# Optimization experiments

Hardware: AMD Instinct MI355X
Metric: run time of the kernel (lower is better)

Reference implementation:

```python
import jax, jax.numpy as jnp
import numpy as np

B, T, C, H = 8, 2048, 1024, 64  # batch, seq (block_size), n_embd, head_size


def setup_inputs() -> dict:
    key = jax.random.key(0)
    kx, kq, kk, kv = jax.random.split(key, 4)
    s = 1.0 / np.sqrt(C)
    return {
        "x": jax.random.normal(kx, (B, T, C), dtype=jnp.float32),
        "Wq": jax.random.normal(kq, (C, H), dtype=jnp.float32) * s,
        "Wk": jax.random.normal(kk, (C, H), dtype=jnp.float32) * s,
        "Wv": jax.random.normal(kv, (C, H), dtype=jnp.float32) * s,
    }


def reference(x, Wq, Wk, Wv):
    t = x.shape[1]
    q = jnp.einsum("btc,ch->bth", x, Wq)
    k = jnp.einsum("btc,ch->bth", x, Wk)
    v = jnp.einsum("btc,ch->bth", x, Wv)
    scores = jnp.einsum("bqh,bkh->bqk", q, k) / jnp.sqrt(jnp.float32(H))
    causal = jnp.tril(jnp.ones((t, t), dtype=bool))  # tril mask
    scores = jnp.where(causal, scores, -jnp.inf)
    attn = jax.nn.softmax(scores, axis=-1)
    return jnp.einsum("bqk,bkh->bqh", attn, v)
```

## Files before the change

### kernel.cpp

```cpp
#include <hip/hip_runtime.h>
#include <hip/hip_bf16.h>

#define BB 8
#define TT 2048
#define CC 1024
#define HH 64
#define NSPLIT 8

typedef __attribute__((ext_vector_type(8)))  short bf16x8;
typedef __attribute__((ext_vector_type(4)))  float f32x4;
typedef __attribute__((ext_vector_type(16))) float f32x16;
typedef __attribute__((ext_vector_type(8)))  unsigned short us8;
typedef unsigned int u32;

static __device__ __forceinline__ unsigned short f2bf(float f) {
    union { float f; unsigned int u; } v; v.f = f;
    unsigned int u = v.u;
    return (unsigned short)((u + 0x7FFFu + ((u >> 16) & 1u)) >> 16);
}
static __device__ __forceinline__ float bf2f(unsigned short s) {
    union { u32 u; float f; } v; v.u = ((u32)s) << 16; return v.f;
}

__global__ __launch_bounds__(256) void prep_weights(
        const float* __restrict__ Wq, const float* __restrict__ Wk,
        const float* __restrict__ Wv, unsigned short* __restrict__ Wt) {
    __shared__ float tile[64][65];
    int w  = blockIdx.x >> 4;
    int c0 = (blockIdx.x & 15) * 64;
    const float* W = (w == 0) ? Wq : (w == 1) ? Wk : Wv;
    int li = threadIdx.x;
    {
        int c = li >> 2, h4 = (li & 3) * 16;
        const float* src = W + (size_t)(c0 + c) * HH + h4;
        #pragma unroll
        for (int i = 0; i < 4; ++i) {
            float4 v4 = *(const float4*)(src + i * 4);
            tile[c][h4 + i*4 + 0] = v4.x; tile[c][h4 + i*4 + 1] = v4.y;
            tile[c][h4 + i*4 + 2] = v4.z; tile[c][h4 + i*4 + 3] = v4.w;
        }
    }
    __syncthreads();
    float scale = (w == 0) ? 0.1803368802f : 1.0f;
    int h = li >> 2, cg = (li & 3) * 16;
    unsigned short* dst = Wt + (size_t)w * HH * CC + (size_t)h * CC + c0 + cg;
    #pragma unroll
    for (int i = 0; i < 16; ++i) dst[i] = f2bf(tile[cg + i][h] * scale);
}

__global__ __launch_bounds__(512, 4) void proj_qkv(
        const float* __restrict__ x, const unsigned short* __restrict__ Wt,
        unsigned short* __restrict__ Pp) {
    __shared__ unsigned short Xs[2][64 * 64];
    __shared__ unsigned short Ws[2][192 * 64];
    int tid = threadIdx.x;
    int wv = tid >> 6, lane = tid & 63;
    int quad = (lane >> 4) & 3, lq = lane & 15;
    int mg = wv >> 2, ng = wv & 3;
    int r0 = blockIdx.x * 64;
    int k0 = blockIdx.y * 512;

    int xr = tid >> 3, xg = tid & 7;
    const float* xsrc = x + (size_t)(r0 + xr) * CC + k0 + xg * 8;
    int xdst = xr * 64 + ((xg ^ (xr & 7)) * 8);
    float4 xa[2], xb[2];

    f32x4 acc[2][3];
    #pragma unroll
    for (int mt = 0; mt < 2; ++mt)
        #pragma unroll
        for (int nt = 0; nt < 3; ++nt)
            #pragma unroll
            for (int i = 0; i < 4; ++i) acc[mt][nt][i] = 0.0f;

    auto stageW = [&](int buf, int kc) {
        #pragma unroll
        for (int i = 0; i < 3; ++i) {
            int fp = tid + i * 512;
            int r = fp >> 3, pb = fp & 7, g = pb ^ (r & 7);
            const u32 __attribute__((address_space(1)))* gsrc =
                (const u32 __attribute__((address_space(1)))*)
                    (Wt + (size_t)r * CC + k0 + kc * 64 + g * 8);
            u32 __attribute__((address_space(3)))* ldst =
                (u32 __attribute__((address_space(3)))*)(&Ws[buf][fp * 8]);
            __builtin_amdgcn_global_load_lds(gsrc, ldst, 16, 0, 0);
        }
    };
    auto loadX = [&](int set, int kc) {
        xa[set] = *(const float4*)(xsrc + kc * 64);
        xb[set] = *(const float4*)(xsrc + kc * 64 + 4);
    };
    auto writeX = [&](int set, int buf) {
        unsigned short h[8];
        h[0]=f2bf(xa[set].x); h[1]=f2bf(xa[set].y);
        h[2]=f2bf(xa[set].z); h[3]=f2bf(xa[set].w);
        h[4]=f2bf(xb[set].x); h[5]=f2bf(xb[set].y);
        h[6]=f2bf(xb[set].z); h[7]=f2bf(xb[set].w);
        *(us8*)&Xs[buf][xdst] = *(const us8*)h;
    };

    loadX(0, 0); loadX(1, 1);
    stageW(0, 0);
    writeX(0, 0);

    for (int kc = 0; kc < 8; ++kc) {
        int cur = kc & 1;
        __syncthreads();
        if (kc < 7) stageW(1 - cur, kc + 1);
        if (kc < 6) loadX(kc & 1, kc + 2);
        #pragma unroll
        for (int ks = 0; ks < 2; ++ks) {
            int g = ks * 4 + quad;
            bf16x8 a[2], b[3];
            #pragma unroll
            for (int mt = 0; mt < 2; ++mt) {
                int arow = mg * 32 + mt * 16 + lq;
                a[mt] = *(const bf16x8*)&Xs[cur][arow * 64 + (g ^ (lq & 7)) * 8];
            }
            #pragma unroll
            for (int nt = 0; nt < 3; ++nt) {
                int brow = ng * 48 + nt * 16 + lq;
                b[nt] = *(const bf16x8*)&Ws[cur][brow * 64 + (g ^ (lq & 7)) * 8];
            }
            #pragma unroll
            for (int mt = 0; mt < 2; ++mt)
                #pragma unroll
                for (int nt = 0; nt < 3; ++nt)
                    acc[mt][nt] = __builtin_amdgcn_mfma_f32_16x16x32_bf16(
                        a[mt], b[nt], acc[mt][nt], 0, 0, 0);
        }
        if (kc < 7) writeX((kc + 1) & 1, 1 - cur);
    }

    unsigned short* Pb =
        Pp + ((size_t)blockIdx.y * (BB * TT) + r0) * 192;
    #pragma unroll
    for (int mt = 0; mt < 2; ++mt) {
        #pragma unroll
        for (int nt = 0; nt < 3; ++nt) {
            int g = ng * 48 + nt * 16 + lq;
            #pragma unroll
            for (int i = 0; i < 4; ++i) {
                int row = mg * 32 + mt * 16 + quad * 4 + i;
                Pb[(size_t)row * 192 + g] = f2bf(acc[mt][nt][i]);
            }
        }
    }
}

__global__ __launch_bounds__(256) void qkv_reduce(
        const unsigned short* __restrict__ Pp,
        unsigned short* __restrict__ qws, unsigned short* __restrict__ kws,
        unsigned short* __restrict__ vws) {
    __shared__ unsigned short Vt[64][72];
    int t = threadIdx.x;
    int br0 = blockIdx.x * 64;
    const size_t H2 = (size_t)BB * TT * 192;
    {
        int r = br0 + (t >> 2), cg = (t & 3) * 32;
        const unsigned short* p0 = Pp + (size_t)r * 192 + cg;
        const unsigned short* p1 = p0 + H2;
        unsigned short* dst = (cg < 64) ? (qws + (size_t)r * HH + cg)
                                        : (kws + (size_t)r * HH + (cg - 64));
        #pragma unroll
        for (int u = 0; u < 4; ++u) {
            us8 a = *(const us8*)(p0 + u * 8);
            us8 b = *(const us8*)(p1 + u * 8);
            unsigned short o[8];
            #pragma unroll
            for (int j = 0; j < 8; ++j) o[j] = f2bf(bf2f(a[j]) + bf2f(b[j]));
            *(us8*)(dst + u * 8) = *(const us8*)o;
        }
    }
    {
        int r = br0 + (t >> 2), ch = (t & 3) * 16;
        const unsigned short* p0 = Pp + (size_t)r * 192 + 128 + ch;
        const unsigned short* p1 = p0 + H2;
        #pragma unroll
        for (int u = 0; u < 2; ++u) {
            us8 a = *(const us8*)(p0 + u * 8);
            us8 b = *(const us8*)(p1 + u * 8);
            #pragma unroll
            for (int j = 0; j < 8; ++j)
                Vt[ch + u * 8 + j][r & 63] = f2bf(bf2f(a[j]) + bf2f(b[j]));
        }
    }
    __syncthreads();
    {
        int h = t >> 2, tb = (t & 3) * 16;
        int b = br0 >> 11, rr = br0 & (TT - 1);
        #pragma unroll
        for (int u = 0; u < 2; ++u)
            *(us8*)(vws + ((size_t)b * HH + h) * TT + rr + tb + u * 8) =
                *(const us8*)&Vt[h][tb + u * 8];
    }
}

__global__ __launch_bounds__(128, 3) void attn(
        const unsigned short* __restrict__ qws,
        const unsigned short* __restrict__ kws,
        const unsigned short* __restrict__ vws,
        unsigned short* __restrict__ Op, float* __restrict__ Lp) {
    __shared__ unsigned short Kt[32][72];
    __shared__ unsigned short Vt[64][40];
    __shared__ unsigned short Ps[64][40];
    int ti = blockIdx.x;
    int s  = blockIdx.y;
    int b  = blockIdx.z;
    int last = 2 * ti + 1;
    if (s > last) return;
    int tid = threadIdx.x, wv = tid >> 6, lane = tid & 63;
    int half = lane >> 5, l31 = lane & 31;

    bf16x8 qf[4];
    {
        const unsigned short* qp =
            qws + ((size_t)b * TT + ti * 64 + wv * 32 + l31) * HH + half * 8;
        #pragma unroll
        for (int ks = 0; ks < 4; ++ks) qf[ks] = *(const bf16x8*)(qp + ks * 16);
    }
    f32x16 O0, O1, Lc;
    #pragma unroll
    for (int i = 0; i < 16; ++i) { O0[i] = 0.f; O1[i] = 0.f; Lc[i] = 0.f; }
    bf16x8 ones;
    #pragma unroll
    for (int i = 0; i < 8; ++i) ones[i] = (short)0x3F80;

    for (int jc = s; jc <= last; jc += NSPLIT) {
        __syncthreads();
        #pragma unroll
        for (int i = 0; i < 2; ++i) {
            int slot = tid + i * 128;
            int r = slot >> 3, g = slot & 7;
            *(us8*)&Kt[r][g * 8] =
                *(const us8*)(kws + ((size_t)b * TT + jc * 32 + r) * HH + g * 8);
        }
        #pragma unroll
        for (int i = 0; i < 2; ++i) {
            int slot = tid + i * 128;
            int h = slot >> 2, kb = slot & 3;
            *(us8*)&Vt[h][kb * 8] =
                *(const us8*)(vws + ((size_t)b * HH + h) * TT + jc * 32 + kb * 8);
        }
        __syncthreads();
        f32x16 S;
        #pragma unroll
        for (int i = 0; i < 16; ++i) S[i] = 0.f;
        #pragma unroll
        for (int ks = 0; ks < 4; ++ks) {
            bf16x8 kf = *(const bf16x8*)&Kt[l31][ks * 16 + half * 8];
            S = __builtin_amdgcn_mfma_f32_32x32x16_bf16(qf[ks], kf, S, 0, 0, 0);
        }
        bool diag = (jc >= 2 * ti + wv);
        #pragma unroll
        for (int r = 0; r < 16; ++r) {
            int pat = (r & 3) + 8 * (r >> 2) + 4 * half;
            float p = __builtin_amdgcn_exp2f(S[r]);
            if (diag && jc * 32 + l31 > ti * 64 + wv * 32 + pat) p = 0.0f;
            Ps[wv * 32 + pat][l31] = f2bf(p);
        }
        #pragma unroll
        for (int ks = 0; ks < 2; ++ks) {
            bf16x8 pa  = *(const bf16x8*)&Ps[wv * 32 + l31][ks * 16 + half * 8];
            bf16x8 vf0 = *(const bf16x8*)&Vt[l31][ks * 16 + half * 8];
            bf16x8 vf1 = *(const bf16x8*)&Vt[32 + l31][ks * 16 + half * 8];
            O0 = __builtin_amdgcn_mfma_f32_32x32x16_bf16(pa, vf0, O0, 0, 0, 0);
            O1 = __builtin_amdgcn_mfma_f32_32x32x16_bf16(pa, vf1, O1, 0, 0, 0);
            Lc = __builtin_amdgcn_mfma_f32_32x32x16_bf16(pa, ones, Lc, 0, 0, 0);
        }
    }
    unsigned short* Ob =
        Op + (((size_t)s * BB + b) * TT + ti * 64 + wv * 32) * HH;
    #pragma unroll
    for (int r = 0; r < 16; ++r) {
        int pat = (r & 3) + 8 * (r >> 2) + 4 * half;
        Ob[(size_t)pat * HH + l31]      = f2bf(O0[r]);
        Ob[(size_t)pat * HH + 32 + l31] = f2bf(O1[r]);
    }
    if (l31 == 0) {
        #pragma unroll
        for (int r = 0; r < 16; ++r) {
            int pat = (r & 3) + 8 * (r >> 2) + 4 * half;
            Lp[((size_t)s * BB + b) * TT + ti * 64 + wv * 32 + pat] = Lc[r];
        }
    }
}

__global__ __launch_bounds__(256) void norm_out(
        const unsigned short* __restrict__ Op, const float* __restrict__ Lp,
        float* __restrict__ out) {
    int idx = blockIdx.x * 256 + threadIdx.x;
    int g = idx >> 2;
    int hseg = (idx & 3) * 16;
    int ti = (g & (TT - 1)) >> 6;
    int ns = min(2 * ti + 2, NSPLIT);
    float a[16];
    #pragma unroll
    for (int j = 0; j < 16; ++j) a[j] = 0.f;
    float Ls = 0.f;
    for (int s = 0; s < ns; ++s) {
        const unsigned short* base =
            Op + ((size_t)s * BB * TT + g) * HH + hseg;
        us8 u0 = *(const us8*)base;
        us8 u1 = *(const us8*)(base + 8);
        #pragma unroll
        for (int j = 0; j < 8; ++j) { a[j] += bf2f(u0[j]); a[8 + j] += bf2f(u1[j]); }
        Ls += Lp[(size_t)s * BB * TT + g];
    }
    float inv = 1.0f / Ls;
    float* ob = out + (size_t)g * HH + hseg;
    #pragma unroll
    for (int q = 0; q < 4; ++q) {
        float4 v = make_float4(a[q*4] * inv, a[q*4+1] * inv,
                               a[q*4+2] * inv, a[q*4+3] * inv);
        ((float4*)ob)[q] = v;
    }
}

extern "C" void kernel_launch(void* const* d_in, const int* in_sizes, int n_in,
                              void* d_out, int out_size, void* d_ws, size_t ws_size,
                              hipStream_t stream) {
    (void)in_sizes; (void)n_in; (void)out_size; (void)ws_size;
    const float* x  = (const float*)d_in[0];
    const float* Wq = (const float*)d_in[1];
    const float* Wk = (const float*)d_in[2];
    const float* Wv = (const float*)d_in[3];
    float* out = (float*)d_out;

    char* ws = (char*)d_ws;
    unsigned short* Wt  = (unsigned short*)ws;
    unsigned short* qws = (unsigned short*)(ws + (1u << 19));
    unsigned short* kws = (unsigned short*)(ws + (1u << 19) + (1u << 21));
    unsigned short* vws = (unsigned short*)(ws + (1u << 19) + (2u << 21));
    unsigned short* Op  = (unsigned short*)(ws + (1u << 19) + (3u << 21));
    float*          Lp  = (float*)(ws + (1u << 19) + (3u << 21) + (1u << 24));
    unsigned short* Pp  = (unsigned short*)(ws + (1u << 19) + (3u << 21)
                                            + (1u << 24) + (1u << 19));

    prep_weights<<<48, 256, 0, stream>>>(Wq, Wk, Wv, Wt);
    proj_qkv<<<dim3(256, 2), 512, 0, stream>>>(x, Wt, Pp);
    qkv_reduce<<<256, 256, 0, stream>>>(Pp, qws, kws, vws);
    attn<<<dim3(32, NSPLIT, 8), 128, 0, stream>>>(qws, kws, vws, Op, Lp);
    norm_out<<<256, 256, 0, stream>>>(Op, Lp, out);
}
```

Measured before the change: 136.9 us.

## Double-buffer 64-key K/V tiles via async global-to-LDS loads with swizzled layout

The attention kernel now processes 64-key tiles instead of 32, and halves the split count. K and V are prefetched into double-buffered shared memory with global_load_lds, so copies overlap with MFMA work. qkv_reduce writes K and V in an XOR-swizzled, tile-blocked layout so the shared-memory fragment reads avoid bank conflicts. Occupancy drops to two blocks per SM to fit the larger shared buffers. There is a risk: the async LDS loads may not be fully waited on before the barrier.

```diff
diff --git a/kernel.cpp b/kernel.cpp
--- a/kernel.cpp
+++ b/kernel.cpp
@@ -5,7 +5,7 @@
 #define TT 2048
 #define CC 1024
 #define HH 64
-#define NSPLIT 8
+#define NSPLIT 4
 
 typedef __attribute__((ext_vector_type(8)))  short bf16x8;
 typedef __attribute__((ext_vector_type(4)))  float f32x4;
@@ -160,8 +160,6 @@
         int r = br0 + (t >> 2), cg = (t & 3) * 32;
         const unsigned short* p0 = Pp + (size_t)r * 192 + cg;
         const unsigned short* p1 = p0 + H2;
-        unsigned short* dst = (cg < 64) ? (qws + (size_t)r * HH + cg)
-                                        : (kws + (size_t)r * HH + (cg - 64));
         #pragma unroll
         for (int u = 0; u < 4; ++u) {
             us8 a = *(const us8*)(p0 + u * 8);
@@ -169,7 +167,13 @@
             unsigned short o[8];
             #pragma unroll
             for (int j = 0; j < 8; ++j) o[j] = f2bf(bf2f(a[j]) + bf2f(b[j]));
-            *(us8*)(dst + u * 8) = *(const us8*)o;
+            if (cg < 64) {
+                *(us8*)(qws + (size_t)r * HH + cg + u * 8) = *(const us8*)o;
+            } else {
+                int gb = ((cg - 64) >> 3) + u;
+                int pb = gb ^ (r & 7);
+                *(us8*)(kws + (size_t)r * HH + pb * 8) = *(const us8*)o;
+            }
         }
     }
     {
@@ -188,27 +192,28 @@
     __syncthreads();
     {
         int h = t >> 2, tb = (t & 3) * 16;
-        int b = br0 >> 11, rr = br0 & (TT - 1);
-        #pragma unroll
-        for (int u = 0; u < 2; ++u)
-            *(us8*)(vws + ((size_t)b * HH + h) * TT + rr + tb + u * 8) =
-                *(const us8*)&Vt[h][tb + u * 8];
-    }
-}
-
-__global__ __launch_bounds__(128, 3) void attn(
+        int b = br0 >> 11, jc = (br0 & (TT - 1)) >> 6;
+        unsigned short* base = vws + (((size_t)b * 32 + jc) * 64 + h) * 64;
+        #pragma unroll
+        for (int u = 0; u < 2; ++u) {
+            int gb = (t & 3) * 2 + u;
+            int pb = gb ^ (h & 7);
+            *(us8*)(base + pb * 8) = *(const us8*)&Vt[h][tb + u * 8];
+        }
+    }
+}
+
+__global__ __launch_bounds__(128, 2) void attn(
         const unsigned short* __restrict__ qws,
         const unsigned short* __restrict__ kws,
         const unsigned short* __restrict__ vws,
         unsigned short* __restrict__ Op, float* __restrict__ Lp) {
-    __shared__ unsigned short Kt[32][72];
-    __shared__ unsigned short Vt[64][40];
-    __shared__ unsigned short Ps[64][40];
+    __shared__ unsigned short KV[16384 + 64 * 66];
+    unsigned short* Ps = &KV[16384];
     int ti = blockIdx.x;
     int s  = blockIdx.y;
     int b  = blockIdx.z;
-    int last = 2 * ti + 1;
-    if (s > last) return;
+    if (s > ti) return;
     int tid = threadIdx.x, wv = tid >> 6, lane = tid & 63;
     int half = lane >> 5, l31 = lane & 31;
 
@@ -226,48 +231,65 @@
     #pragma unroll
     for (int i = 0; i < 8; ++i) ones[i] = (short)0x3F80;
 
-    for (int jc = s; jc <= last; jc += NSPLIT) {
+    auto stageKV = [&](int buf, int jc) {
+        const unsigned short* kbase = kws + ((size_t)b * TT + jc * 64) * HH;
+        const unsigned short* vbase = vws + (((size_t)b * 32 + jc) * 64) * 64;
+        #pragma unroll
+        for (int u = 0; u < 4; ++u) {
+            int f = u * 128 + tid;
+            const u32 __attribute__((address_space(1)))* gk =
+                (const u32 __attribute__((address_space(1)))*)(kbase + f * 8);
+            u32 __attribute__((address_space(3)))* lk =
+                (u32 __attribute__((address_space(3)))*)(&KV[buf * 4096 + f * 8]);
+            __builtin_amdgcn_global_load_lds(gk, lk, 16, 0, 0);
+            const u32 __attribute__((address_space(1)))* gv =
+                (const u32 __attribute__((address_space(1)))*)(vbase + f * 8);
+            u32 __attribute__((address_space(3)))* lv =
+                (u32 __attribute__((address_space(3)))*)(&KV[8192 + buf * 4096 + f * 8]);
+            __builtin_amdgcn_global_load_lds(gv, lv, 16, 0, 0);
+        }
+    };
+
+    stageKV(0, s);
+    int buf = 0;
+    for (int jc = s; jc <= ti; jc += NSPLIT) {
         __syncthreads();
-        #pragma unroll
-        for (int i = 0; i < 2; ++i) {
-            int slot = tid + i * 128;
-            int r = slot >> 3, g = slot & 7;
-            *(us8*)&Kt[r][g * 8] =
-                *(const us8*)(kws + ((size_t)b * TT + jc * 32 + r) * HH + g * 8);
-        }
-        #pragma unroll
-        for (int i = 0; i < 2; ++i) {
-            int slot = tid + i * 128;
-            int h = slot >> 2, kb = slot & 3;
-            *(us8*)&Vt[h][kb * 8] =
-                *(const us8*)(vws + ((size_t)b * HH + h) * TT + jc * 32 + kb * 8);
-        }
-        __syncthreads();
-        f32x16 S;
-        #pragma unroll
-        for (int i = 0; i < 16; ++i) S[i] = 0.f;
+        if (jc + NSPLIT <= ti) stageKV(1 - buf, jc + NSPLIT);
+        const unsigned short* Kc = &KV[buf * 4096];
+        const unsigned short* Vc = &KV[8192 + buf * 4096];
+        f32x16 S[2];
+        #pragma unroll
+        for (int i = 0; i < 16; ++i) { S[0][i] = 0.f; S[1][i] = 0.f; }
+        #pragma unroll
+        for (int nt = 0; nt < 2; ++nt)
+            #pragma unroll
+            for (int ks = 0; ks < 4; ++ks) {
+                int row = nt * 32 + l31, gb = ks * 2 + half;
+                bf16x8 kf = *(const bf16x8*)&Kc[row * 64 + (gb ^ (row & 7)) * 8];
+                S[nt] = __builtin_amdgcn_mfma_f32_32x32x16_bf16(
+                    qf[ks], kf, S[nt], 0, 0, 0);
+            }
+        bool diag = (jc == ti);
+        #pragma unroll
+        for (int nt = 0; nt < 2; ++nt)
+            #pragma unroll
+            for (int r = 0; r < 16; ++r) {
+                int pat = (r & 3) + 8 * (r >> 2) + 4 * half;
+                float p = __builtin_amdgcn_exp2f(S[nt][r]);
+                if (diag && nt * 32 + l31 > wv * 32 + pat) p = 0.0f;
+                Ps[(wv * 32 + pat) * 66 + nt * 32 + l31] = f2bf(p);
+            }
         #pragma unroll
         for (int ks = 0; ks < 4; ++ks) {
-            bf16x8 kf = *(const bf16x8*)&Kt[l31][ks * 16 + half * 8];
-            S = __builtin_amdgcn_mfma_f32_32x32x16_bf16(qf[ks], kf, S, 0, 0, 0);
-        }
-        bool diag = (jc >= 2 * ti + wv);
-        #pragma unroll
-        for (int r = 0; r < 16; ++r) {
-            int pat = (r & 3) + 8 * (r >> 2) + 4 * half;
-            float p = __builtin_amdgcn_exp2f(S[r]);
-            if (diag && jc * 32 + l31 > ti * 64 + wv * 32 + pat) p = 0.0f;
-            Ps[wv * 32 + pat][l31] = f2bf(p);
-        }
-        #pragma unroll
-        for (int ks = 0; ks < 2; ++ks) {
-            bf16x8 pa  = *(const bf16x8*)&Ps[wv * 32 + l31][ks * 16 + half * 8];
-            bf16x8 vf0 = *(const bf16x8*)&Vt[l31][ks * 16 + half * 8];
-            bf16x8 vf1 = *(const bf16x8*)&Vt[32 + l31][ks * 16 + half * 8];
+            int gb = ks * 2 + half;
+            bf16x8 pa = *(const bf16x8*)&Ps[(wv * 32 + l31) * 66 + ks * 16 + half * 8];
+            bf16x8 vf0 = *(const bf16x8*)&Vc[l31 * 64 + (gb ^ (l31 & 7)) * 8];
+            bf16x8 vf1 = *(const bf16x8*)&Vc[(32 + l31) * 64 + (gb ^ (l31 & 7)) * 8];
             O0 = __builtin_amdgcn_mfma_f32_32x32x16_bf16(pa, vf0, O0, 0, 0, 0);
             O1 = __builtin_amdgcn_mfma_f32_32x32x16_bf16(pa, vf1, O1, 0, 0, 0);
             Lc = __builtin_amdgcn_mfma_f32_32x32x16_bf16(pa, ones, Lc, 0, 0, 0);
         }
+        buf = 1 - buf;
     }
     unsigned short* Ob =
         Op + (((size_t)s * BB + b) * TT + ti * 64 + wv * 32) * HH;
@@ -293,7 +315,7 @@
     int g = idx >> 2;
     int hseg = (idx & 3) * 16;
     int ti = (g & (TT - 1)) >> 6;
-    int ns = min(2 * ti + 2, NSPLIT);
+    int ns = min(ti + 1, NSPLIT);
     float a[16];
     #pragma unroll
     for (int j = 0; j < 16; ++j) a[j] = 0.f;
```

Result: slower. 145.2 us (+6.1%).
